# Performance work log

Hardware: AMD Instinct MI355X
Metric: run time of the kernel (lower is better)

## Reference

```python
import jax, jax.numpy as jnp
import numpy as np

TK = 3          # number of temporal scales (wavedec level = TK-1)
SK = 3          # spatial rank count per scale (SK-1 rank-1 terms + residual)
INPUT_LEN = 256
N_NODES = 256
K = 32          # randomized-SVD sketch size
INV_SQRT2 = np.float32(1.0 / np.sqrt(2.0))


def haar_wavedec(x, levels):
    # x: (..., L) with L divisible by 2**levels; pywt haar, mode='zero', even L
    # returns [cD1, cD2, ..., cD_levels, cA_levels]  (== pywt.wavedec(...)[::-1])
    coeffs = []
    for _ in range(levels):
        L = x.shape[-1]
        pairs = x.reshape(x.shape[:-1] + (L // 2, 2))
        a, b = pairs[..., 0], pairs[..., 1]
        coeffs.append((a - b) * INV_SQRT2)  # detail cD
        x = (a + b) * INV_SQRT2             # approx cA
    coeffs.append(x)
    return coeffs


def setup_inputs() -> dict:
    key = jax.random.key(0)
    kx, kp = jax.random.split(key)
    x = jax.random.normal(kx, (4, INPUT_LEN, 64, N_NODES), dtype=jnp.float32)
    p = jax.random.normal(kp, (N_NODES, K), dtype=jnp.float32)
    return {"x": x, "p": p}


def reference(x, p):
    # x: (B, T, c, n) -> permute(0,2,3,1) -> (B, c, n, T)
    xw = jnp.transpose(x, (0, 2, 3, 1))
    coeffs = haar_wavedec(xw, TK - 1)  # TK tensors (B, c, n, L_i)
    res = []
    for xi in coeffs:
        if SK == 1:
            res.append(xi)
            continue
        xt = jnp.transpose(xi, (0, 3, 1, 2))          # (B, L, c, n)
        z = xt @ p                                     # (B, L, c, k)
        q, _ = jnp.linalg.qr(z)                        # reduced: (B, L, c, k)
        y = jnp.einsum('blck,blcn->blkn', q, xt)       # (B, L, k, n)
        u, s, vh = jnp.linalg.svd(y, full_matrices=False)  # u:(B,L,k,k) s:(B,L,k) vh:(B,L,k,n)
        u = q @ u                                      # (B, L, c, k)
        # rank-1 terms s_j * u_j v_j^T for j < SK-1, vectorized over j
        terms = jnp.einsum('blcj,blj,bljn->jblcn',
                           u[..., :SK - 1], s[..., :SK - 1], vh[..., :SK - 1, :])
        terms = jnp.transpose(terms, (0, 1, 3, 4, 2))  # (SK-1, B, c, n, L)
        resid = xi - terms.sum(axis=0)
        for j in range(SK - 1):
            res.append(terms[j])
        res.append(resid)
    # left-pad last dim to INPUT_LEN, then stack -> (TK*SK, B, c, n, INPUT_LEN)
    res = [jnp.pad(r, ((0, 0), (0, 0), (0, 0), (INPUT_LEN - r.shape[-1], 0))) for r in res]
    return jnp.stack(res)
```

## Files before the change

### kernel.cpp

```cpp
#include <hip/hip_runtime.h>

#define IS2f 0.70710678118654752440f

#define WS_Z   0ul
#define WS_G   2097152ul
#define WS_H   3145728ul
#define WS_SU  4194304ul
#define WS_VV  4325376ul
#define WS_B   4849664ul

#define WSYNC() asm volatile("" ::: "memory")

__device__ __forceinline__ float frcp(float v){ return __builtin_amdgcn_rcpf(v); }
__device__ __forceinline__ float frsq(float v){ return __builtin_amdgcn_rsqf(v); }
__device__ __forceinline__ float fsq (float v){ return __builtin_amdgcn_sqrtf(v); }
__device__ __forceinline__ float readlane_f(float v, int sl){
  return __uint_as_float(__builtin_amdgcn_readlane(__float_as_uint(v), sl));
}

__device__ __forceinline__ void decode_pid(int pid, int& ci, int& b, int& l, int& L){
  if (pid < 512)      { ci = 0; b = pid >> 7; l = pid & 127; L = 128; }
  else if (pid < 768) { int q = pid - 512; ci = 1; b = q >> 6; l = q & 63; L = 64; }
  else                { int q = pid - 768; ci = 2; b = q >> 6; l = q & 63; L = 64; }
}
__device__ __forceinline__ int su_base(int ci){ return ci==0 ? 0 : (ci==1 ? 65536 : 98304); }
__device__ __forceinline__ int vv_base(int ci){ return ci==0 ? 0 : (ci==1 ? 262144 : 393216); }
__device__ __forceinline__ int tpp(int r, int m){ return (m==0) ? r  : (r+m)%31; }
__device__ __forceinline__ int tqq(int r, int m){ return (m==0) ? 31 : (r+31-m)%31; }

#define PTS 260

__global__ __launch_bounds__(512) void k_fact(const float* __restrict__ x,
                                              const float* __restrict__ p,
                                              float* __restrict__ ws, int storeB){
  __shared__ __align__(16) float Ms[64*256];
  __shared__ __align__(16) float Zs[64*32];
  __shared__ __align__(16) float Pt[32*PTS];
  __shared__ __align__(16) float Bn[32*PTS];
  __shared__ float Gl[33*33];

  int pid = blockIdx.x, tid = threadIdx.x;
  int ci,b,l,L; decode_pid(pid,ci,b,l,L);

  {
    const float4* p4 = (const float4*)p;
    #pragma unroll
    for (int e=0;e<4;++e){
      int idx = tid + 512*e;
      int n = idx >> 3, k4 = idx & 7;
      float4 v = p4[idx];
      Pt[(4*k4+0)*PTS + n] = v.x;
      Pt[(4*k4+1)*PTS + n] = v.y;
      Pt[(4*k4+2)*PTS + n] = v.z;
      Pt[(4*k4+3)*PTS + n] = v.w;
    }
  }
  const float4* x4 = (const float4*)x;
  float4* Ms4 = (float4*)Ms;
  if (ci == 0){
    size_t base = ((size_t)(b*256 + 2*l) * 64) * 64;
    #pragma unroll
    for (int e=0;e<8;++e){
      int f = tid + 512*e;
      float4 A = x4[base + f];
      float4 Bv = x4[base + 4096 + f];
      float4 m;
      m.x=(A.x-Bv.x)*IS2f; m.y=(A.y-Bv.y)*IS2f; m.z=(A.z-Bv.z)*IS2f; m.w=(A.w-Bv.w)*IS2f;
      Ms4[f] = m;
    }
  } else {
    float sg = (ci==1) ? -0.5f : 0.5f;
    size_t base = ((size_t)(b*256 + 4*l) * 64) * 64;
    #pragma unroll
    for (int e=0;e<8;++e){
      int f = tid + 512*e;
      float4 A = x4[base + f];
      float4 B1 = x4[base + 4096 + f];
      float4 C1 = x4[base + 8192 + f];
      float4 D1 = x4[base + 12288 + f];
      float4 m;
      m.x=(A.x+B1.x)*0.5f + (C1.x+D1.x)*sg;
      m.y=(A.y+B1.y)*0.5f + (C1.y+D1.y)*sg;
      m.z=(A.z+B1.z)*0.5f + (C1.z+D1.z)*sg;
      m.w=(A.w+B1.w)*0.5f + (C1.w+D1.w)*sg;
      Ms4[f] = m;
    }
  }
  __syncthreads();

  {
    int k = tid & 31, c0 = tid >> 5;
    float acc[4] = {0,0,0,0};
    for (int n4=0;n4<64;++n4){
      float4 pv = *(const float4*)&Pt[k*PTS + 4*n4];
      #pragma unroll
      for (int i=0;i<4;++i){
        float4 m = Ms4[(c0*4+i)*64 + n4];
        acc[i] += m.x*pv.x + m.y*pv.y + m.z*pv.z + m.w*pv.w;
      }
    }
    #pragma unroll
    for (int i=0;i<4;++i){
      int c = c0*4 + i;
      Zs[c*32+k] = acc[i];
      ws[WS_Z + (size_t)pid*2048 + c*32 + k] = acc[i];
    }
  }
  __syncthreads();

  {
    int kk = tid & 31, j0 = tid >> 5;
    float ga[2] = {0,0};
    for (int c=0;c<64;++c){
      float zk = Zs[c*32+kk];
      #pragma unroll
      for (int e=0;e<2;++e) ga[e] += Zs[c*32 + j0 + 16*e] * zk;
    }
    #pragma unroll
    for (int e=0;e<2;++e)
      Gl[(j0+16*e)*33 + kk] = ga[e];
  }

  {
    int n4 = tid & 63, kg = tid >> 6;
    float4 facc[4];
    #pragma unroll
    for (int kq=0;kq<4;++kq){ facc[kq].x=0.f; facc[kq].y=0.f; facc[kq].z=0.f; facc[kq].w=0.f; }
    for (int c=0;c<64;++c){
      float4 mv = Ms4[c*64 + n4];
      float4 z1 = *(const float4*)&Zs[c*32 + kg*4];
      float zz[4] = {z1.x,z1.y,z1.z,z1.w};
      #pragma unroll
      for (int kq=0;kq<4;++kq){
        facc[kq].x += zz[kq]*mv.x; facc[kq].y += zz[kq]*mv.y;
        facc[kq].z += zz[kq]*mv.z; facc[kq].w += zz[kq]*mv.w;
      }
    }
    #pragma unroll
    for (int kq=0;kq<4;++kq){
      int krow = kg*4 + kq;
      *(float4*)&Bn[krow*PTS + 4*n4] = facc[kq];
      if (storeB)
        *(float4*)&ws[WS_B + (size_t)pid*8192 + (size_t)krow*256 + 4*n4] = facc[kq];
    }
  }
  __syncthreads();

  {
    int jlane = tid & 31, grp = tid >> 5;
    for (int k=0;k<32;++k){
      float gkk  = Gl[k*33+k];
      float ginv = frcp(gkk);
      float gkj  = Gl[k*33+jlane];
      float av[2], bv[2];
      #pragma unroll
      for (int e=0;e<2;++e){
        int i = k+1+grp+16*e; int ii = (i<32)? i : 31;
        av[e] = Gl[ii*33+jlane];
        bv[e] = Gl[k*33+ii];
      }
      WSYNC();
      #pragma unroll
      for (int e=0;e<2;++e){
        int i = k+1+grp+16*e;
        if (i < 32) Gl[i*33+jlane] = av[e] - bv[e]*gkj*ginv;
      }
      __syncthreads();
    }
    float sv[2];
    #pragma unroll
    for (int e=0;e<2;++e){
      int i = grp+16*e;
      sv[e] = Gl[i*33+jlane] * frsq(Gl[i*33+i]);
    }
    WSYNC();
    #pragma unroll
    for (int e=0;e<2;++e){
      int i = grp+16*e;
      Gl[i*33+jlane] = sv[e];
    }
  }
  __syncthreads();

  #pragma unroll
  for (int e=0;e<2;++e){
    int idx = tid + 512*e;
    ws[WS_G + (size_t)pid*1024 + idx] = Gl[(idx>>5)*33 + (idx&31)];
  }

  if (tid < 256){
    int n = tid;
    float c[32];
    #pragma unroll
    for (int i=0;i<32;++i){
      float cv = Bn[i*PTS + n];
      #pragma unroll
      for (int k=0;k<i;++k) cv -= Gl[k*33+i]*c[k];
      c[i] = cv * frcp(Gl[i*33+i]);
    }
    #pragma unroll
    for (int i=0;i<32;++i) Bn[i*PTS + n] = c[i];
  }
  __syncthreads();

  {
    int kk = tid & 31, j0 = tid >> 5;
    float h[2] = {0,0};
    for (int n4=0;n4<64;++n4){
      float4 bk = *(const float4*)&Bn[kk*PTS + 4*n4];
      #pragma unroll
      for (int e=0;e<2;++e){
        float4 bj = *(const float4*)&Bn[(j0+16*e)*PTS + 4*n4];
        h[e] += bj.x*bk.x + bj.y*bk.y + bj.z*bk.z + bj.w*bk.w;
      }
    }
    #pragma unroll
    for (int e=0;e<2;++e)
      ws[WS_H + (size_t)pid*1024 + (j0+16*e)*32 + kk] = h[e];
  }
}

#define NSWEEP 5

__global__ __launch_bounds__(128) void k_solve(const float* __restrict__ x,
                                               float* __restrict__ ws, int useB){
  __shared__ float Gs[32*33];
  __shared__ float Hs[32*33];
  __shared__ float Vsh[32*33];
  __shared__ float cA[16], sA[16];
  __shared__ float ggs[2][32];
  __shared__ float uss[2][64];

  int pid = blockIdx.x, tid = threadIdx.x;
  int wave = tid >> 6;
  int lane = tid & 63;
  int jlane = tid & 31;
  int hlf  = (tid >> 5) & 1;
  int ci,b,l,L; decode_pid(pid,ci,b,l,L);

  #pragma unroll
  for (int e=0;e<8;++e){
    int idx = tid + 128*e; int i = idx>>5, j = idx&31;
    Gs[i*33+j]  = ws[WS_G + (size_t)pid*1024 + idx];
    Hs[i*33+j]  = ws[WS_H + (size_t)pid*1024 + idx];
    Vsh[i*33+j] = (i==j) ? 1.f : 0.f;
  }
  __syncthreads();

  float dmx = (lane < 32) ? fabsf(Hs[jlane*33+jlane]) : 0.f;
  #pragma unroll
  for (int off=1; off<64; off<<=1) dmx = fmaxf(dmx, __shfl_xor(dmx, off));
  float thr = dmx * 3e-6f;

  for (int sw=0; sw<NSWEEP; ++sw){
    for (int r=0; r<31; ++r){
      if (wave == 0){
        int m = lane & 15;
        int pm = tpp(r,m), qm = tqq(r,m);
        float app = Hs[pm*33+pm];
        float aqq = Hs[qm*33+qm];
        float apq = Hs[pm*33+qm];
        if (!__ballot(fabsf(apq) > thr)) continue;
        float tau = (aqq - app) * frcp(2.f*apq);
        float tt  = ((tau>=0.f)?1.f:-1.f) * frcp(fabsf(tau) + fsq(fmaf(tau,tau,1.f)));
        float cc  = frsq(fmaf(tt,tt,1.f));
        float ss  = tt*cc;
        bool ok = fabsf(apq) > 1e-28f;
        if (lane < 16){ cA[lane] = ok?cc:1.f; sA[lane] = ok?ss:0.f; }
        WSYNC();

        int m2 = lane >> 2, lm = lane & 3;
        int p2 = tpp(r,m2), q2 = tqq(r,m2);
        float c2 = cA[m2], s2 = sA[m2];
        float a_[4], b_[4], c_[4], d_[4], c1v[4], s1v[4];
        int p1v[4], q1v[4];
        #pragma unroll
        for (int e=0;e<4;++e){
          int m1 = lm + 4*e;
          int p1 = tpp(r,m1), q1 = tqq(r,m1);
          p1v[e]=p1; q1v[e]=q1;
          c1v[e]=cA[m1]; s1v[e]=sA[m1];
          a_[e] = Hs[p1*33+p2]; b_[e] = Hs[p1*33+q2];
          c_[e] = Hs[q1*33+p2]; d_[e] = Hs[q1*33+q2];
        }
        WSYNC();
        #pragma unroll
        for (int e=0;e<4;++e){
          float c1 = c1v[e], s1 = s1v[e];
          float a1 = c1*a_[e] - s1*c_[e];
          float b1 = c1*b_[e] - s1*d_[e];
          float c1r= s1*a_[e] + c1*c_[e];
          float d1 = s1*b_[e] + c1*d_[e];
          Hs[p1v[e]*33+p2] = c2*a1 - s2*b1;
          Hs[p1v[e]*33+q2] = s2*a1 + c2*b1;
          Hs[q1v[e]*33+p2] = c2*c1r - s2*d1;
          Hs[q1v[e]*33+q2] = s2*c1r + c2*d1;
        }
      } else {
        int m2 = lane >> 2, lm = lane & 3;
        int p2 = tpp(r,m2), q2 = tqq(r,m2);
        float app = Hs[p2*33+p2];
        float aqq = Hs[q2*33+q2];
        float apq = Hs[p2*33+q2];
        if (!__ballot(fabsf(apq) > thr)) continue;
        float tau = (aqq - app) * frcp(2.f*apq);
        float tt  = ((tau>=0.f)?1.f:-1.f) * frcp(fabsf(tau) + fsq(fmaf(tau,tau,1.f)));
        float cc  = frsq(fmaf(tt,tt,1.f));
        float ss  = tt*cc;
        bool ok = fabsf(apq) > 1e-28f;
        float c2 = ok?cc:1.f, s2 = ok?ss:0.f;

        float vp[8], vq[8];
        #pragma unroll
        for (int e=0;e<8;++e){
          int i = lm + 4*e;
          vp[e] = Vsh[i*33+p2];
          vq[e] = Vsh[i*33+q2];
        }
        WSYNC();
        #pragma unroll
        for (int e=0;e<8;++e){
          int i = lm + 4*e;
          Vsh[i*33+p2] = c2*vp[e] - s2*vq[e];
          Vsh[i*33+q2] = s2*vp[e] + c2*vq[e];
        }
      }
      __syncthreads();
    }
  }
  __syncthreads();
  if (wave == 1) return;

  float rdgr = frcp(Gs[jlane*33+jlane]);

  float dv = (lane < 32) ? Hs[jlane*33+jlane] : -3e38f;
  float m1r = dv;
  #pragma unroll
  for (int off=1; off<64; off<<=1) m1r = fmaxf(m1r, __shfl_xor(m1r, off));
  unsigned long long bm = __ballot(dv == m1r);
  int i0 = __ffsll((unsigned long long)bm) - 1;
  float dv2 = (lane == i0) ? -3e38f : dv;
  float m2r = dv2;
  #pragma unroll
  for (int off=1; off<64; off<<=1) m2r = fmaxf(m2r, __shfl_xor(m2r, off));
  unsigned long long bm2 = __ballot(dv2 == m2r);
  int i1 = __ffsll((unsigned long long)bm2) - 1;

  float lam = hlf ? m2r : m1r;
  int   ti  = hlf ? i1 : i0;
  float sj  = fsq(fmaxf(lam, 0.f)); sj = fmaxf(sj, 1e-12f);
  float s0 = readlane_f(sj, 0);
  float s1 = readlane_f(sj, 32);

  {
    float rr = Vsh[jlane*33 + ti];
    float Greg[32];
    #pragma unroll
    for (int i=0;i<32;++i) Greg[i] = Gs[jlane*33+i];
    #pragma unroll
    for (int i=31;i>=0;--i){
      float ri = __shfl(rr,  hlf*32 + i);
      float di = __shfl(rdgr, i);
      float g  = ri * di;
      if (jlane == i) ggs[hlf][i] = g;
      if (jlane < i)  rr -= Greg[i]*g;
    }
  }
  WSYNC();

  {
    const float4* Z4 = (const float4*)(ws + WS_Z + (size_t)pid*2048);
    float u0 = 0.f, u1 = 0.f;
    #pragma unroll
    for (int k4=0;k4<8;++k4){
      float4 z = Z4[lane*8 + k4];
      u0 += z.x*ggs[0][k4*4+0] + z.y*ggs[0][k4*4+1] + z.z*ggs[0][k4*4+2] + z.w*ggs[0][k4*4+3];
      u1 += z.x*ggs[1][k4*4+0] + z.y*ggs[1][k4*4+1] + z.z*ggs[1][k4*4+2] + z.w*ggs[1][k4*4+3];
    }
    uss[0][lane] = u0; uss[1][lane] = u1;
    ws[WS_SU + su_base(ci) + ((size_t)(b*2+0)*64 + lane)*L + l] = s0*u0;
    ws[WS_SU + su_base(ci) + ((size_t)(b*2+1)*64 + lane)*L + l] = s1*u1;
  }
  WSYNC();

  float i0s = frcp(s0), i1s = frcp(s1);
  size_t vb0 = WS_VV + vv_base(ci) + ((size_t)(b*2+0)*L + l)*256 + lane*4;
  size_t vb1 = WS_VV + vv_base(ci) + ((size_t)(b*2+1)*L + l)*256 + lane*4;

  if (useB){
    const float4* B4 = (const float4*)(ws + WS_B + (size_t)pid*8192);
    float a0x=0,a0y=0,a0z=0,a0w=0, a1x=0,a1y=0,a1z=0,a1w=0;
    #pragma unroll 8
    for (int k=0;k<32;++k){
      float4 bv = B4[(size_t)k*64 + lane];
      float g0 = ggs[0][k], g1 = ggs[1][k];
      a0x += g0*bv.x; a0y += g0*bv.y; a0z += g0*bv.z; a0w += g0*bv.w;
      a1x += g1*bv.x; a1y += g1*bv.y; a1z += g1*bv.z; a1w += g1*bv.w;
    }
    float4 r0; r0.x=a0x*i0s; r0.y=a0y*i0s; r0.z=a0z*i0s; r0.w=a0w*i0s;
    float4 r1; r1.x=a1x*i1s; r1.y=a1y*i1s; r1.z=a1z*i1s; r1.w=a1w*i1s;
    *(float4*)(ws + vb0) = r0;
    *(float4*)(ws + vb1) = r1;
  } else {
    float a0x=0,a0y=0,a0z=0,a0w=0, a1x=0,a1y=0,a1z=0,a1w=0;
    const float4* x4 = (const float4*)x;
    if (ci == 0){
      size_t base = ((size_t)(b*256 + 2*l) * 64) * 64;
      #pragma unroll 2
      for (int c=0;c<64;++c){
        float4 A  = x4[base + c*64 + lane];
        float4 Bv = x4[base + 4096 + c*64 + lane];
        float mx=(A.x-Bv.x)*IS2f, my=(A.y-Bv.y)*IS2f, mz=(A.z-Bv.z)*IS2f, mw=(A.w-Bv.w)*IS2f;
        float uc0 = uss[0][c], uc1 = uss[1][c];
        a0x += uc0*mx; a0y += uc0*my; a0z += uc0*mz; a0w += uc0*mw;
        a1x += uc1*mx; a1y += uc1*my; a1z += uc1*mz; a1w += uc1*mw;
      }
    } else {
      float sg = (ci==1) ? -0.5f : 0.5f;
      size_t base = ((size_t)(b*256 + 4*l) * 64) * 64;
      #pragma unroll 2
      for (int c=0;c<64;++c){
        float4 A  = x4[base + c*64 + lane];
        float4 B1 = x4[base + 4096 + c*64 + lane];
        float4 C1 = x4[base + 8192 + c*64 + lane];
        float4 D1 = x4[base + 12288 + c*64 + lane];
        float mx=(A.x+B1.x)*0.5f + (C1.x+D1.x)*sg;
        float my=(A.y+B1.y)*0.5f + (C1.y+D1.y)*sg;
        float mz=(A.z+B1.z)*0.5f + (C1.z+D1.z)*sg;
        float mw=(A.w+B1.w)*0.5f + (C1.w+D1.w)*sg;
        float uc0 = uss[0][c], uc1 = uss[1][c];
        a0x += uc0*mx; a0y += uc0*my; a0z += uc0*mz; a0w += uc0*mw;
        a1x += uc1*mx; a1y += uc1*my; a1z += uc1*mz; a1w += uc1*mw;
      }
    }
    ws[vb0+0]=a0x*i0s; ws[vb0+1]=a0y*i0s; ws[vb0+2]=a0z*i0s; ws[vb0+3]=a0w*i0s;
    ws[vb1+0]=a1x*i1s; ws[vb1+1]=a1y*i1s; ws[vb1+2]=a1z*i1s; ws[vb1+3]=a1w*i1s;
  }
}

__global__ __launch_bounds__(256) void k_out(const float* __restrict__ x,
                                             const float* __restrict__ ws,
                                             float* __restrict__ out){
  __shared__ float d1[128*33];
  __shared__ float d2[64*33];
  __shared__ float a2s[64*33];
  __shared__ float Vs[2*128*33];
  __shared__ float Us[512];

  int nt = blockIdx.x, c = blockIdx.y, b = blockIdx.z;
  int n0 = nt * 32, tid = threadIdx.x;
  float* a1 = Vs;

  const float4* x4 = (const float4*)x;
  #pragma unroll
  for (int e=0;e<4;++e){
    int f = tid + 256*e; int l1 = f>>3, d4 = f&7;
    size_t r = ((size_t)(b*256 + 2*l1)*64 + c)*64 + (n0>>2) + d4;
    float4 A = x4[r], Bv = x4[r + 4096];
    int o = l1*33 + 4*d4;
    d1[o+0]=(A.x-Bv.x)*IS2f; d1[o+1]=(A.y-Bv.y)*IS2f; d1[o+2]=(A.z-Bv.z)*IS2f; d1[o+3]=(A.w-Bv.w)*IS2f;
    a1[o+0]=(A.x+Bv.x)*IS2f; a1[o+1]=(A.y+Bv.y)*IS2f; a1[o+2]=(A.z+Bv.z)*IS2f; a1[o+3]=(A.w+Bv.w)*IS2f;
  }
  __syncthreads();
  #pragma unroll
  for (int e=0;e<2;++e){
    int f = tid + 256*e; int l2 = f>>3, d4 = f&7;
    #pragma unroll
    for (int j=0;j<4;++j){
      int dn = 4*d4 + j;
      float aa = a1[(2*l2)*33 + dn], bb = a1[(2*l2+1)*33 + dn];
      d2[l2*33+dn]  = (aa-bb)*IS2f;
      a2s[l2*33+dn] = (aa+bb)*IS2f;
    }
  }
  #pragma unroll
  for (int e=0;e<2;++e){
    int idx = tid + 256*e;
    int j, l, L, so;
    if (idx < 256)      { j=idx>>7;        l=idx&127; L=128; so=0; }
    else if (idx < 384) { j=(idx-256)>>6;  l=idx&63;  L=64;  so=65536; }
    else                { j=(idx-384)>>6;  l=idx&63;  L=64;  so=98304; }
    Us[idx] = ws[WS_SU + so + ((size_t)(b*2+j)*64 + c)*L + l];
  }
  __syncthreads();

  for (int cc=0; cc<3; ++cc){
    int L   = (cc==0) ? 128 : 64;
    int pad = 256 - L;
    int sb  = cc*3;
    int uo  = (cc==0) ? 0 : (cc==1) ? 256 : 384;
    const float* cf = (cc==0) ? d1 : (cc==1) ? d2 : a2s;

    int iters = (2*L*32) >> 8;
    for (int e=0;e<iters;++e){
      int idx = tid + 256*e;
      int j = (idx >= L*32) ? 1 : 0;
      int rem = idx - j*L*32;
      int ll = rem >> 5, dn = rem & 31;
      Vs[j*4224 + ll*33 + dn] =
        ws[WS_VV + vv_base(cc) + ((size_t)(b*2+j)*L + ll)*256 + n0 + dn];
    }
    __syncthreads();

    int l = tid - pad;
    bool inr = (l >= 0);
    size_t obase = (size_t)sb*16777216 + (size_t)b*4194304 + (size_t)c*65536
                 + (size_t)n0*256 + tid;
    #pragma unroll 4
    for (int dn=0; dn<32; ++dn){
      float v0 = 0.f, v1 = 0.f, rv = 0.f;
      if (inr){
        float q0 = Us[uo + l]     * Vs[l*33 + dn];
        float q1 = Us[uo + L + l] * Vs[4224 + l*33 + dn];
        v0 = q0; v1 = q1;
        rv = cf[l*33 + dn] - q0 - q1;
      }
      out[obase + dn*256]            = v0;
      out[obase + dn*256 + 16777216] = v1;
      out[obase + dn*256 + 33554432] = rv;
    }
    __syncthreads();
  }
}

extern "C" void kernel_launch(void* const* d_in, const int* in_sizes, int n_in,
                              void* d_out, int out_size, void* d_ws, size_t ws_size,
                              hipStream_t stream) {
  const float* x = (const float*)d_in[0];
  const float* p = (const float*)d_in[1];
  float* out = (float*)d_out;
  float* ws  = (float*)d_ws;

  int useB = (ws_size >= (size_t)(WS_B + 1024ull*8192ull) * 4ull) ? 1 : 0;

  k_fact <<<1024, 512, 0, stream>>>(x, p, ws, useB);
  k_solve<<<1024, 128, 0, stream>>>(x, ws, useB);
  k_out  <<<dim3(8,64,4), 256, 0, stream>>>(x, ws, out);
}
```

Before: 448.1 us.

## Split Jacobi H and V rotations evenly across both waves with transposed V

In k_solve, the Jacobi eigen-solve used to give wave 0 all H updates and wave 1 all V updates. Now each wave computes the rotation parameters redundantly, and each wave applies half of the 16 column-pair rotations to both H and V. V is stored transposed with stride 36, so each rotation updates rows with float4 accesses. The change balances the work between the two waves and vectorises the V updates, at the cost of an extra __syncthreads per rotation step between reads and writes.

```diff
diff --git a/kernel.cpp b/kernel.cpp
--- a/kernel.cpp
+++ b/kernel.cpp
@@ -27,6 +27,16 @@
 __device__ __forceinline__ int vv_base(int ci){ return ci==0 ? 0 : (ci==1 ? 262144 : 393216); }
 __device__ __forceinline__ int tpp(int r, int m){ return (m==0) ? r  : (r+m)%31; }
 __device__ __forceinline__ int tqq(int r, int m){ return (m==0) ? 31 : (r+31-m)%31; }
+__device__ __forceinline__ void jparam(float app, float aqq, float apq,
+                                       float& cc, float& ss){
+  float tau = (aqq - app) * frcp(2.f*apq);
+  float tt  = ((tau>=0.f)?1.f:-1.f) * frcp(fabsf(tau) + fsq(fmaf(tau,tau,1.f)));
+  float c   = frsq(fmaf(tt,tt,1.f));
+  float s   = tt*c;
+  bool ok = fabsf(apq) > 1e-28f;
+  cc = ok ? c : 1.f;
+  ss = ok ? s : 0.f;
+}
 
 #define PTS 260
 
@@ -226,8 +236,8 @@
                                                float* __restrict__ ws, int useB){
   __shared__ float Gs[32*33];
   __shared__ float Hs[32*33];
-  __shared__ float Vsh[32*33];
-  __shared__ float cA[16], sA[16];
+  __shared__ __align__(16) float Vt[32*36];
+  __shared__ float cA2[2][16], sA2[2][16];
   __shared__ float ggs[2][32];
   __shared__ float uss[2][64];
 
@@ -243,8 +253,11 @@
     int idx = tid + 128*e; int i = idx>>5, j = idx&31;
     Gs[i*33+j]  = ws[WS_G + (size_t)pid*1024 + idx];
     Hs[i*33+j]  = ws[WS_H + (size_t)pid*1024 + idx];
-    Vsh[i*33+j] = (i==j) ? 1.f : 0.f;
-  }
+  }
+  #pragma unroll
+  for (int e=0;e<9;++e) Vt[tid + 128*e] = 0.f;
+  __syncthreads();
+  if (tid < 32) Vt[tid*36 + tid] = 1.f;
   __syncthreads();
 
   float dmx = (lane < 32) ? fabsf(Hs[jlane*33+jlane]) : 0.f;
@@ -252,79 +265,59 @@
   for (int off=1; off<64; off<<=1) dmx = fmaxf(dmx, __shfl_xor(dmx, off));
   float thr = dmx * 3e-6f;
 
+  float4* Vt4 = (float4*)Vt;
+  int m2 = (lane >> 3) + 8*wave;
+  int g  = lane & 7;
+
   for (int sw=0; sw<NSWEEP; ++sw){
     for (int r=0; r<31; ++r){
-      if (wave == 0){
-        int m = lane & 15;
-        int pm = tpp(r,m), qm = tqq(r,m);
-        float app = Hs[pm*33+pm];
-        float aqq = Hs[qm*33+qm];
-        float apq = Hs[pm*33+qm];
-        if (!__ballot(fabsf(apq) > thr)) continue;
-        float tau = (aqq - app) * frcp(2.f*apq);
-        float tt  = ((tau>=0.f)?1.f:-1.f) * frcp(fabsf(tau) + fsq(fmaf(tau,tau,1.f)));
-        float cc  = frsq(fmaf(tt,tt,1.f));
-        float ss  = tt*cc;
-        bool ok = fabsf(apq) > 1e-28f;
-        if (lane < 16){ cA[lane] = ok?cc:1.f; sA[lane] = ok?ss:0.f; }
-        WSYNC();
-
-        int m2 = lane >> 2, lm = lane & 3;
-        int p2 = tpp(r,m2), q2 = tqq(r,m2);
-        float c2 = cA[m2], s2 = sA[m2];
-        float a_[4], b_[4], c_[4], d_[4], c1v[4], s1v[4];
-        int p1v[4], q1v[4];
-        #pragma unroll
-        for (int e=0;e<4;++e){
-          int m1 = lm + 4*e;
-          int p1 = tpp(r,m1), q1 = tqq(r,m1);
-          p1v[e]=p1; q1v[e]=q1;
-          c1v[e]=cA[m1]; s1v[e]=sA[m1];
-          a_[e] = Hs[p1*33+p2]; b_[e] = Hs[p1*33+q2];
-          c_[e] = Hs[q1*33+p2]; d_[e] = Hs[q1*33+q2];
-        }
-        WSYNC();
-        #pragma unroll
-        for (int e=0;e<4;++e){
-          float c1 = c1v[e], s1 = s1v[e];
-          float a1 = c1*a_[e] - s1*c_[e];
-          float b1 = c1*b_[e] - s1*d_[e];
-          float c1r= s1*a_[e] + c1*c_[e];
-          float d1 = s1*b_[e] + c1*d_[e];
-          Hs[p1v[e]*33+p2] = c2*a1 - s2*b1;
-          Hs[p1v[e]*33+q2] = s2*a1 + c2*b1;
-          Hs[q1v[e]*33+p2] = c2*c1r - s2*d1;
-          Hs[q1v[e]*33+q2] = s2*c1r + c2*d1;
-        }
-      } else {
-        int m2 = lane >> 2, lm = lane & 3;
-        int p2 = tpp(r,m2), q2 = tqq(r,m2);
-        float app = Hs[p2*33+p2];
-        float aqq = Hs[q2*33+q2];
-        float apq = Hs[p2*33+q2];
-        if (!__ballot(fabsf(apq) > thr)) continue;
-        float tau = (aqq - app) * frcp(2.f*apq);
-        float tt  = ((tau>=0.f)?1.f:-1.f) * frcp(fabsf(tau) + fsq(fmaf(tau,tau,1.f)));
-        float cc  = frsq(fmaf(tt,tt,1.f));
-        float ss  = tt*cc;
-        bool ok = fabsf(apq) > 1e-28f;
-        float c2 = ok?cc:1.f, s2 = ok?ss:0.f;
-
-        float vp[8], vq[8];
-        #pragma unroll
-        for (int e=0;e<8;++e){
-          int i = lm + 4*e;
-          vp[e] = Vsh[i*33+p2];
-          vq[e] = Vsh[i*33+q2];
-        }
-        WSYNC();
-        #pragma unroll
-        for (int e=0;e<8;++e){
-          int i = lm + 4*e;
-          Vsh[i*33+p2] = c2*vp[e] - s2*vq[e];
-          Vsh[i*33+q2] = s2*vp[e] + c2*vq[e];
-        }
-      }
+      int m = lane & 15;
+      int pm = tpp(r,m), qm = tqq(r,m);
+      float apq = Hs[pm*33+qm];
+      if (!__ballot(fabsf(apq) > thr)) continue;
+      float app = Hs[pm*33+pm];
+      float aqq = Hs[qm*33+qm];
+      float cc, ssv; jparam(app, aqq, apq, cc, ssv);
+      if (lane < 16){ cA2[wave][lane] = cc; sA2[wave][lane] = ssv; }
+      WSYNC();
+
+      int p2 = tpp(r,m2), q2 = tqq(r,m2);
+      float c2 = cA2[wave][m2], s2 = sA2[wave][m2];
+
+      float a_[2], b_[2], c_[2], d_[2], c1v[2], s1v[2];
+      int p1v[2], q1v[2];
+      #pragma unroll
+      for (int e=0;e<2;++e){
+        int m1 = g + 8*e;
+        int p1 = tpp(r,m1), q1 = tqq(r,m1);
+        p1v[e]=p1; q1v[e]=q1;
+        c1v[e]=cA2[wave][m1]; s1v[e]=sA2[wave][m1];
+        a_[e] = Hs[p1*33+p2]; b_[e] = Hs[p1*33+q2];
+        c_[e] = Hs[q1*33+p2]; d_[e] = Hs[q1*33+q2];
+      }
+      float4 vp = Vt4[p2*9 + g];
+      float4 vq = Vt4[q2*9 + g];
+      __syncthreads();
+
+      #pragma unroll
+      for (int e=0;e<2;++e){
+        float c1 = c1v[e], s1 = s1v[e];
+        float a1 = c1*a_[e] - s1*c_[e];
+        float b1 = c1*b_[e] - s1*d_[e];
+        float c1r= s1*a_[e] + c1*c_[e];
+        float d1 = s1*b_[e] + c1*d_[e];
+        Hs[p1v[e]*33+p2] = c2*a1 - s2*b1;
+        Hs[p1v[e]*33+q2] = s2*a1 + c2*b1;
+        Hs[q1v[e]*33+p2] = c2*c1r - s2*d1;
+        Hs[q1v[e]*33+q2] = s2*c1r + c2*d1;
+      }
+      float4 np, nq;
+      np.x = c2*vp.x - s2*vq.x;  nq.x = s2*vp.x + c2*vq.x;
+      np.y = c2*vp.y - s2*vq.y;  nq.y = s2*vp.y + c2*vq.y;
+      np.z = c2*vp.z - s2*vq.z;  nq.z = s2*vp.z + c2*vq.z;
+      np.w = c2*vp.w - s2*vq.w;  nq.w = s2*vp.w + c2*vq.w;
+      Vt4[p2*9 + g] = np;
+      Vt4[q2*9 + g] = nq;
       __syncthreads();
     }
   }
@@ -353,7 +346,7 @@
   float s1 = readlane_f(sj, 32);
 
   {
-    float rr = Vsh[jlane*33 + ti];
+    float rr = Vt[ti*36 + jlane];
     float Greg[32];
     #pragma unroll
     for (int i=0;i<32;++i) Greg[i] = Gs[jlane*33+i];
```

Result: faster. 426.1 us (-4.9%).
